# Optimization experiments

Hardware: AMD Instinct MI355X
Metric: run time of the kernel (lower is better)

Reference implementation:

```python
import jax, jax.numpy as jnp
import numpy as np

T, N, FIN, HID, E = 3, 50000, 4, 128, 1600000
EPS = 1e-5


def setup_inputs() -> dict:
    key = jax.random.key(0)
    ks = jax.random.split(key, 16)
    s = 0.05
    return {
        "X": jax.random.normal(ks[0], (T, N, FIN), jnp.float32),
        "edge_index": jax.random.randint(ks[1], (2, E), 0, N, jnp.int64),
        "edge_weight": jax.random.uniform(ks[2], (E,), jnp.float32),
        "w1": jax.random.normal(ks[3], (FIN, HID), jnp.float32) * s,
        "wc": jax.random.normal(ks[4], (3, HID, HID), jnp.float32) * s,
        "bc": jnp.zeros((4, HID), jnp.float32),
        "bn_gamma": jnp.ones((4, HID), jnp.float32),
        "bn_beta": jnp.zeros((4, HID), jnp.float32),
        "lstm_wih": jax.random.normal(ks[5], (2, 4 * HID, HID), jnp.float32) * s,
        "lstm_whh": jax.random.normal(ks[6], (2, 4 * HID, HID), jnp.float32) * s,
        "lstm_b": jnp.zeros((2, 4 * HID), jnp.float32),
        "lin1_w": jax.random.normal(ks[7], (HID + T, HID), jnp.float32) * s,
        "lin1_b": jnp.zeros((HID,), jnp.float32),
        "lin2_w": jax.random.normal(ks[8], (HID, 1), jnp.float32) * s,
        "lin2_b": jnp.zeros((1,), jnp.float32),
    }


def reference(X, edge_index, edge_weight, w1, wc, bc, bn_gamma, bn_beta,
              lstm_wih, lstm_whh, lstm_b, lin1_w, lin1_b, lin2_w, lin2_b):
    n = X.shape[1]
    src, dst = edge_index[0], edge_index[1]
    loop = jnp.arange(n)
    # PyG gcn_norm: add self loops (weight 1), symmetric normalization
    src_a = jnp.concatenate([src, loop])
    dst_a = jnp.concatenate([dst, loop])
    w_a = jnp.concatenate([edge_weight, jnp.ones((n,), X.dtype)])
    deg = jax.ops.segment_sum(w_a, dst_a, num_segments=n)
    dinv = jnp.where(deg > 0, deg ** -0.5, 0.0)
    norm = dinv[src_a] * w_a * dinv[dst_a]  # [E+N]

    def gcn(x, w, b):
        h = x @ w                                   # [N,H] transform first (F small)
        msg = h[src_a] * norm[:, None]              # gather + scale
        return jax.ops.segment_sum(msg, dst_a, num_segments=n) + b

    def bn(h, g, beta):  # BatchNorm1d with batch stats (track_running_stats=False)
        mu = h.mean(0)
        var = ((h - mu) ** 2).mean(0)
        return (h - mu) / jnp.sqrt(var + EPS) * g + beta

    def per_timestep(x):
        h = bn(jax.nn.relu(gcn(x, w1, bc[0])), bn_gamma[0], bn_beta[0])
        for i in range(3):
            h = bn(jax.nn.relu(gcn(h, wc[i], bc[i + 1])), bn_gamma[i + 1], bn_beta[i + 1])
        return h

    C = jax.vmap(per_timestep)(X)  # [T, N, H]

    def lstm_layer(seq, wih, whh, b):
        hdim = whh.shape[1]
        h0 = jnp.zeros((seq.shape[1], hdim), seq.dtype)

        def step(carry, x):
            h, c = carry
            gates = x @ wih.T + h @ whh.T + b
            i, f, g, o = jnp.split(gates, 4, axis=-1)  # torch gate order i,f,g,o
            c = jax.nn.sigmoid(f) * c + jax.nn.sigmoid(i) * jnp.tanh(g)
            h = jax.nn.sigmoid(o) * jnp.tanh(c)
            return (h, c), h

        (hT, _), ys = jax.lax.scan(step, (h0, h0), seq)
        return ys, hT

    seq = C
    for layer in range(2):
        seq, hT = lstm_layer(seq, lstm_wih[layer], lstm_whh[layer], lstm_b[layer])

    h = jax.nn.relu(hT)                 # last layer's final hidden, [N, H]
    S = X[:, :, 0].T                    # [N, T]
    h = jnp.concatenate([h, S], axis=-1)
    h = h @ lin1_w + lin1_b
    h = h @ lin2_w + lin2_b             # dropout is identity at inference
    return h
```

## Files before the change

### kernel.cpp

```cpp
#include <hip/hip_runtime.h>
#include <hip/hip_fp8.h>
#include <cstdint>

#define TT  3
#define FIN 4
#define HID 128
#define RS16 384
#define RS32 192
#define RS8  384

typedef unsigned int   u32;
typedef unsigned short u16;
typedef unsigned char  u8;
typedef unsigned long long u64;
typedef float f32x2 __attribute__((ext_vector_type(2)));
typedef float f32x4 __attribute__((ext_vector_type(4)));
typedef __bf16 bf16x8 __attribute__((ext_vector_type(8)));

static __device__ __forceinline__ f32x4 mfma_bf16(bf16x8 a, bf16x8 b, f32x4 c) {
  return __builtin_amdgcn_mfma_f32_16x16x32_bf16(a, b, c, 0, 0, 0);
}
static __device__ __forceinline__ float sigf(float v) { return 1.f / (1.f + expf(-v)); }
static __device__ __forceinline__ float bf_lo(u32 u) { return __uint_as_float(u << 16); }
static __device__ __forceinline__ float bf_hi(u32 u) { return __uint_as_float(u & 0xffff0000u); }
static __device__ __forceinline__ u16 bfbits(float f) {
  return __builtin_bit_cast(unsigned short, (__bf16)f);
}
static __device__ __forceinline__ u8 f_to_fp8(float f) {
  __hip_fp8_e4m3 v(f); return (u8)v.__x;
}
static __device__ __forceinline__ f32x2 fp8x2_to_f32(u16 x) {
  return __builtin_amdgcn_cvt_pk_f32_fp8((int)(u32)x, false);
}


__global__ void k_init(u64* pk, float* stats, int* ticket, int n) {
  int i = blockIdx.x * 256 + threadIdx.x;
  if (i < n) pk[i] = 0ull;
  if (blockIdx.x == 0) {
    for (int k = 0; k < 3; ++k) stats[k * 256 + threadIdx.x] = 0.f;
    if (threadIdx.x == 0) *ticket = 0;
  }
}

__global__ void k_deg(const int* __restrict__ dstv, const float* __restrict__ ew,
                      u64* pk, int* __restrict__ epos, int E_) {
  int e = blockIdx.x * 256 + threadIdx.x;
  if (e < E_) {
    int d = dstv[e];
    u64 inc = (1ull << 42) | (u64)(ew[e] * 4294967296.0f);
    u64 old = atomicAdd(&pk[d], inc);
    epos[e] = (int)(old >> 42);
  }
}

__global__ __launch_bounds__(256) void k_scanA(const u64* __restrict__ pk, int* rowptr,
    int* partial, float* dinv, float* selfn, int n) {
  __shared__ int wsum[4];
  int tid = threadIdx.x, lane = tid & 63, wv = tid >> 6;
  int i = blockIdx.x * 256 + tid;
  int v = 0;
  if (i < n) {
    u64 p = pk[i];
    v = (int)(p >> 42);
    float degw = (float)((double)(p & ((1ull << 42) - 1)) * (1.0 / 4294967296.0) + 1.0);
    float r = rsqrtf(degw);
    dinv[i] = r; selfn[i] = r * r;
  }
  int inc = v;
  #pragma unroll
  for (int off = 1; off < 64; off <<= 1) {
    int t2 = __shfl_up(inc, off);
    if (lane >= off) inc += t2;
  }
  if (lane == 63) wsum[wv] = inc;
  __syncthreads();
  if (tid == 0) {
    int s = 0;
    #pragma unroll
    for (int j = 0; j < 4; ++j) { int t3 = wsum[j]; wsum[j] = s; s += t3; }
    partial[blockIdx.x] = s;
  }
  __syncthreads();
  int excl = wsum[wv] + inc - v;
  if (i <= n) rowptr[i] = excl;
}

__global__ __launch_bounds__(256) void k_scanB(int* partial, int nb) {
  __shared__ int wsum[4];
  int tid = threadIdx.x, lane = tid & 63, wv = tid >> 6;
  int v = (tid < nb) ? partial[tid] : 0;
  int inc = v;
  #pragma unroll
  for (int off = 1; off < 64; off <<= 1) {
    int t2 = __shfl_up(inc, off);
    if (lane >= off) inc += t2;
  }
  if (lane == 63) wsum[wv] = inc;
  __syncthreads();
  if (tid == 0) {
    int s = 0;
    #pragma unroll
    for (int j = 0; j < 4; ++j) { int t3 = wsum[j]; wsum[j] = s; s += t3; }
  }
  __syncthreads();
  int excl = wsum[wv] + inc - v;
  if (tid < nb) partial[tid] = excl;
}

__global__ void k_scanC(int* rowptr, const int* __restrict__ partial, int n) {
  int i = blockIdx.x * 256 + threadIdx.x;
  if (i <= n) rowptr[i] += partial[blockIdx.x];
}

__global__ void k_fillcsr(const int* __restrict__ srcv, const int* __restrict__ dstv,
                          const float* __restrict__ ew, const float* __restrict__ dinv,
                          const int* __restrict__ rowptr, const int* __restrict__ epos,
                          int2* __restrict__ csr, int E_) {
  int e = blockIdx.x * 256 + threadIdx.x;
  if (e < E_) {
    int d = dstv[e], s = srcv[e];
    int idx = rowptr[d] + epos[e];
    csr[idx] = make_int2(s, __float_as_int(dinv[s] * ew[e] * dinv[d]));
  }
}


__global__ __launch_bounds__(256) void k_aggX(const float* __restrict__ X,
    const int* __restrict__ rowptr, const int2* __restrict__ csr,
    const float* __restrict__ selfn, float* __restrict__ XA, int N_) {
  int wv = threadIdx.x >> 6, l = threadIdx.x & 63;
  int wid = blockIdx.x * 4 + wv, nw = gridDim.x * 4;
  for (int n = wid; n < N_; n += nw) {
    float acc[12];
    #pragma unroll
    for (int i = 0; i < 12; ++i) acc[i] = 0.f;
    int e0 = rowptr[n], e1 = rowptr[n + 1];
    for (int e = e0 + l; e < e1; e += 64) {
      int2 v2 = csr[e];
      int s = v2.x; float wn = __int_as_float(v2.y);
      #pragma unroll
      for (int t = 0; t < TT; ++t) {
        float4 v = *(const float4*)(X + ((size_t)t * N_ + s) * FIN);
        acc[t*4+0] += wn * v.x; acc[t*4+1] += wn * v.y;
        acc[t*4+2] += wn * v.z; acc[t*4+3] += wn * v.w;
      }
    }
    #pragma unroll
    for (int i = 0; i < 12; ++i)
      for (int off = 32; off; off >>= 1) acc[i] += __shfl_down(acc[i], off);
    if (l == 0) {
      float sn = selfn[n];
      #pragma unroll
      for (int t = 0; t < TT; ++t) {
        float4 v = *(const float4*)(X + ((size_t)t * N_ + n) * FIN);
        XA[(size_t)n*12 + t*4+0] = acc[t*4+0] + sn * v.x;
        XA[(size_t)n*12 + t*4+1] = acc[t*4+1] + sn * v.y;
        XA[(size_t)n*12 + t*4+2] = acc[t*4+2] + sn * v.z;
        XA[(size_t)n*12 + t*4+3] = acc[t*4+3] + sn * v.w;
      }
    }
  }
}

__global__ void k_l0c(const float* __restrict__ XA, const float* __restrict__ w1,
                      const float* __restrict__ bc0, u32* __restrict__ out32, int N_) {
  int tid = blockIdx.x * 256 + threadIdx.x;
  if (tid >= N_ * 64) return;
  int n = tid >> 6, l = tid & 63, cp = 2 * l;
  float w00 = w1[cp],       w01 = w1[cp+1];
  float w10 = w1[HID+cp],   w11 = w1[HID+cp+1];
  float w20 = w1[2*HID+cp], w21 = w1[2*HID+cp+1];
  float w30 = w1[3*HID+cp], w31 = w1[3*HID+cp+1];
  float b0 = bc0[cp], b1 = bc0[cp+1];
  const float* xa = XA + (size_t)n * 12;
  u32* orow = out32 + (size_t)n * RS32 + l;
  #pragma unroll
  for (int t = 0; t < TT; ++t) {
    float4 x = *(const float4*)(xa + t * 4);
    float v0 = fmaxf(b0 + x.x*w00 + x.y*w10 + x.z*w20 + x.w*w30, 0.f);
    float v1 = fmaxf(b1 + x.x*w01 + x.y*w11 + x.z*w21 + x.w*w31, 0.f);
    orow[t * 64] = (u32)bfbits(v0) | ((u32)bfbits(v1) << 16);
  }
}


__global__ __launch_bounds__(256) void k_stats3(const u32* __restrict__ H32, float* stats,
    int* ticket, const float* __restrict__ gamma, const float* __restrict__ beta,
    float* aff , int N_) {
  __shared__ float red[256][12];
  __shared__ int lastf;
  int l = threadIdx.x & 63, half = threadIdx.x >> 6;
  float s1[TT][2] = {}, s2[TT][2] = {};
  for (int n = blockIdx.x * 4 + half; n < N_; n += gridDim.x * 4) {
    const u32* row = H32 + (size_t)n * RS32 + l;
    #pragma unroll
    for (int t = 0; t < TT; ++t) {
      u32 u = row[t * 64];
      float v0 = bf_lo(u), v1 = bf_hi(u);
      s1[t][0] += v0; s2[t][0] += v0 * v0;
      s1[t][1] += v1; s2[t][1] += v1 * v1;
    }
  }
  #pragma unroll
  for (int t = 0; t < TT; ++t) {
    red[threadIdx.x][t*4+0] = s1[t][0]; red[threadIdx.x][t*4+1] = s2[t][0];
    red[threadIdx.x][t*4+2] = s1[t][1]; red[threadIdx.x][t*4+3] = s2[t][1];
  }
  __syncthreads();
  if (half == 0) {
    #pragma unroll
    for (int t = 0; t < TT; ++t) {
      float a0 = 0, a1 = 0, a2 = 0, a3 = 0;
      #pragma unroll
      for (int h2 = 0; h2 < 4; ++h2) {
        a0 += red[h2*64 + l][t*4+0]; a1 += red[h2*64 + l][t*4+1];
        a2 += red[h2*64 + l][t*4+2]; a3 += red[h2*64 + l][t*4+3];
      }
      atomicAdd(&stats[t*256 + 2*l], a0);       atomicAdd(&stats[t*256 + 128 + 2*l], a1);
      atomicAdd(&stats[t*256 + 2*l + 1], a2);   atomicAdd(&stats[t*256 + 128 + 2*l + 1], a3);
    }
  }
  __syncthreads();
  if (threadIdx.x == 0) {
    __threadfence();
    int tk = __hip_atomic_fetch_add(ticket, 1, __ATOMIC_ACQ_REL, __HIP_MEMORY_SCOPE_AGENT);
    lastf = (tk == (int)gridDim.x - 1) ? 1 : 0;
  }
  __syncthreads();
  if (lastf) {
    float invn = 1.f / (float)N_;
    for (int i = threadIdx.x; i < 384; i += 256) {
      int t = i >> 7, c = i & 127;
      float s1v = __hip_atomic_load(&stats[t*256 + c],       __ATOMIC_RELAXED, __HIP_MEMORY_SCOPE_AGENT);
      float s2v = __hip_atomic_load(&stats[t*256 + 128 + c], __ATOMIC_RELAXED, __HIP_MEMORY_SCOPE_AGENT);
      float mu = s1v * invn;
      float var = fmaxf(s2v * invn - mu * mu, 0.f);
      float a = gamma[c] * rsqrtf(var + 1e-5f);
      aff[t*256 + c] = a;
      aff[t*256 + 128 + c] = beta[c] - mu * a;
      stats[t*256 + c] = 0.f; stats[t*256 + 128 + c] = 0.f;
    }
    if (threadIdx.x == 0) *ticket = 0;
  }
}


__global__ void k_swzall(const float* __restrict__ wc, const float* __restrict__ wih,
                         const float* __restrict__ whh,
                         bf16x8* __restrict__ wcsw, bf16x8* __restrict__ wstk) {
  int id = blockIdx.x * 256 + threadIdx.x;
  if (id < 6144) {
    int i = id >> 11, lid = id & 2047;
    int l = lid & 63, frag = lid >> 6;
    int cb = frag & 7, kb = frag >> 3;
    int col = cb * 16 + (l & 15);
    int k0 = kb * 32 + (l >> 4) * 8;
    const float* W = wc + (size_t)i * HID * HID;
    bf16x8 v;
    #pragma unroll
    for (int j = 0; j < 8; ++j) v[j] = (__bf16)W[(size_t)(k0 + j) * HID + col];
    wcsw[i * 2048 + lid] = v;
  } else if (id < 6144 + 32768) {
    int id2 = id - 6144;
    int layer = id2 >> 14, lid = id2 & 16383;
    int l = lid & 63, frag = lid >> 6;
    int cb = frag & 31, kb = frag >> 5;
    int col = cb * 16 + (l & 15);
    int k0 = kb * 32 + (l >> 4) * 8;
    const float* wi = wih + (size_t)layer * 512 * HID;
    const float* wh = whh + (size_t)layer * 512 * HID;
    bf16x8 v;
    #pragma unroll
    for (int j = 0; j < 8; ++j) {
      int k = k0 + j;
      float val = (k < HID) ? wi[(size_t)col * HID + k] : wh[(size_t)col * HID + (k - HID)];
      v[j] = (__bf16)val;
    }
    wstk[layer * 16384 + lid] = v;
  }
}

__global__ void k_headprep(const float* __restrict__ l1w, const float* __restrict__ l1b,
                           const float* __restrict__ l2w, const float* __restrict__ l2b,
                           float* __restrict__ hw) {
  int k = threadIdx.x;
  if (k < HID + TT) {
    float s = 0.f;
    for (int j = 0; j < HID; ++j) s += l1w[(size_t)k * HID + j] * l2w[j];
    hw[k] = s;
  } else if (k == HID + TT) {
    float s = l2b[0];
    for (int j = 0; j < HID; ++j) s += l1b[j] * l2w[j];
    hw[HID + TT] = s;
  }
}


__global__ __launch_bounds__(256) void k_trans3(const u16* __restrict__ Xin,
    const float* __restrict__ aff, const bf16x8* __restrict__ wsw,
    u8* __restrict__ Y, int nblk, int N_) {
  int w = threadIdx.x >> 6, l = threadIdx.x & 63;
  int lr = l & 15, lk = l >> 4;
  int t = blockIdx.x / nblk;
  int blk = blockIdx.x - t * nblk;
  int rbase = blk * 64 + w * 16;
  int arow = rbase + lr;
  bool av = arow < N_;
  const float* fa = aff + t * 256;
  const float* fb = fa + 128;
  f32x4 acc[8];
  #pragma unroll
  for (int cb = 0; cb < 8; ++cb) acc[cb] = (f32x4){0.f, 0.f, 0.f, 0.f};
  #pragma unroll
  for (int kb = 0; kb < 4; ++kb) {
    int ko = kb * 32 + lk * 8;
    bf16x8 af;
    if (av) {
      uint4 u = *(const uint4*)(Xin + (size_t)arow * RS16 + t * 128 + ko);
      float4 a0 = *(const float4*)(fa + ko), a1 = *(const float4*)(fa + ko + 4);
      float4 b0 = *(const float4*)(fb + ko), b1 = *(const float4*)(fb + ko + 4);
      af[0] = (__bf16)(bf_lo(u.x) * a0.x + b0.x);
      af[1] = (__bf16)(bf_hi(u.x) * a0.y + b0.y);
      af[2] = (__bf16)(bf_lo(u.y) * a0.z + b0.z);
      af[3] = (__bf16)(bf_hi(u.y) * a0.w + b0.w);
      af[4] = (__bf16)(bf_lo(u.z) * a1.x + b1.x);
      af[5] = (__bf16)(bf_hi(u.z) * a1.y + b1.y);
      af[6] = (__bf16)(bf_lo(u.w) * a1.z + b1.z);
      af[7] = (__bf16)(bf_hi(u.w) * a1.w + b1.w);
    } else {
      #pragma unroll
      for (int j = 0; j < 8; ++j) af[j] = (__bf16)0.f;
    }
    #pragma unroll
    for (int cb = 0; cb < 8; ++cb) {
      bf16x8 bf = wsw[(kb * 8 + cb) * 64 + l];
      acc[cb] = mfma_bf16(af, bf, acc[cb]);
    }
  }
  #pragma unroll
  for (int cb = 0; cb < 8; ++cb)
    #pragma unroll
    for (int i2 = 0; i2 < 4; ++i2) {
      int orow = rbase + lk * 4 + i2;
      if (orow < N_)
        Y[(size_t)orow * RS8 + t * 128 + cb * 16 + lr] = f_to_fp8(acc[cb][i2]);
    }
}


__global__ __launch_bounds__(256) void k_agg3(const u8* __restrict__ H8,
    const int* __restrict__ rowptr, const int2* __restrict__ csr,
    const float* __restrict__ selfn, const float* __restrict__ bias,
    u16* __restrict__ outp, int N_) {
  int wv = threadIdx.x >> 6, l = threadIdx.x & 63;
  int wid = blockIdx.x * 4 + wv, nw = gridDim.x * 4;
  float b0 = bias[2 * l], b1 = bias[2 * l + 1];
  u32* O32 = (u32*)outp;
  for (int n = wid; n < N_; n += nw) {
    const u16* self = (const u16*)(H8 + (size_t)n * RS8) + l;
    float sn = selfn[n];
    f32x2 v0 = fp8x2_to_f32(self[0]);
    f32x2 v1 = fp8x2_to_f32(self[64]);
    f32x2 v2 = fp8x2_to_f32(self[128]);
    float a00 = sn * v0.x, a01 = sn * v0.y;
    float a10 = sn * v1.x, a11 = sn * v1.y;
    float a20 = sn * v2.x, a21 = sn * v2.y;
    int e0 = rowptr[n], e1 = rowptr[n + 1];
    int e = e0;
    for (; e + 7 < e1; e += 8) {
      int2 c[8];
      #pragma unroll
      for (int j = 0; j < 8; ++j) c[j] = csr[e + j];
      u16 x[8][3];
      #pragma unroll
      for (int j = 0; j < 8; ++j) {
        const u16* p = (const u16*)(H8 + (size_t)c[j].x * RS8) + l;
        x[j][0] = p[0]; x[j][1] = p[64]; x[j][2] = p[128];
      }
      #pragma unroll
      for (int j = 0; j < 8; ++j) {
        float w = __int_as_float(c[j].y);
        f32x2 y0 = fp8x2_to_f32(x[j][0]);
        f32x2 y1 = fp8x2_to_f32(x[j][1]);
        f32x2 y2 = fp8x2_to_f32(x[j][2]);
        a00 += w * y0.x; a01 += w * y0.y;
        a10 += w * y1.x; a11 += w * y1.y;
        a20 += w * y2.x; a21 += w * y2.y;
      }
    }
    for (; e < e1; ++e) {
      int2 c0 = csr[e];
      const u16* p = (const u16*)(H8 + (size_t)c0.x * RS8) + l;
      float w = __int_as_float(c0.y);
      f32x2 y0 = fp8x2_to_f32(p[0]);
      f32x2 y1 = fp8x2_to_f32(p[64]);
      f32x2 y2 = fp8x2_to_f32(p[128]);
      a00 += w * y0.x; a01 += w * y0.y;
      a10 += w * y1.x; a11 += w * y1.y;
      a20 += w * y2.x; a21 += w * y2.y;
    }
    u32* orow = O32 + (size_t)n * RS32 + l;
    orow[0]   = (u32)bfbits(fmaxf(a00 + b0, 0.f)) | ((u32)bfbits(fmaxf(a01 + b1, 0.f)) << 16);
    orow[64]  = (u32)bfbits(fmaxf(a10 + b0, 0.f)) | ((u32)bfbits(fmaxf(a11 + b1, 0.f)) << 16);
    orow[128] = (u32)bfbits(fmaxf(a20 + b0, 0.f)) | ((u32)bfbits(fmaxf(a21 + b1, 0.f)) << 16);
  }
}


__global__ __launch_bounds__(256) void k_lstm(
    const u16* __restrict__ xb, int xs, const u16* __restrict__ hpb,
    const float* __restrict__ aff,
    float* __restrict__ cstate, u16* __restrict__ hout,
    const bf16x8* __restrict__ wsw, const float* __restrict__ bias,
    int first, int N_) {
  __shared__ __bf16 gl[32][512];
  int w = threadIdx.x >> 6, l = threadIdx.x & 63;
  int lr = l & 15, lk = l >> 4;
  int r0 = blockIdx.x * 32;
  f32x4 acc[2][8];
  #pragma unroll
  for (int rb = 0; rb < 2; ++rb)
    #pragma unroll
    for (int cb = 0; cb < 8; ++cb) acc[rb][cb] = (f32x4){0.f, 0.f, 0.f, 0.f};

  #pragma unroll
  for (int kb = 0; kb < 4; ++kb) {
    int ko = kb * 32 + lk * 8;
    bf16x8 af[2];
    #pragma unroll
    for (int rb = 0; rb < 2; ++rb) {
      int row = r0 + rb * 16 + lr;
      if (row < N_) {
        uint4 u = *(const uint4*)(xb + (size_t)row * xs + ko);
        if (aff) {
          float4 a0 = *(const float4*)(aff + ko),       a1 = *(const float4*)(aff + ko + 4);
          float4 b0 = *(const float4*)(aff + HID + ko), b1 = *(const float4*)(aff + HID + ko + 4);
          af[rb][0] = (__bf16)(bf_lo(u.x) * a0.x + b0.x);
          af[rb][1] = (__bf16)(bf_hi(u.x) * a0.y + b0.y);
          af[rb][2] = (__bf16)(bf_lo(u.y) * a0.z + b0.z);
          af[rb][3] = (__bf16)(bf_hi(u.y) * a0.w + b0.w);
          af[rb][4] = (__bf16)(bf_lo(u.z) * a1.x + b1.x);
          af[rb][5] = (__bf16)(bf_hi(u.z) * a1.y + b1.y);
          af[rb][6] = (__bf16)(bf_lo(u.w) * a1.z + b1.z);
          af[rb][7] = (__bf16)(bf_hi(u.w) * a1.w + b1.w);
        } else {
          af[rb] = __builtin_bit_cast(bf16x8, u);
        }
      } else {
        #pragma unroll
        for (int j = 0; j < 8; ++j) af[rb][j] = (__bf16)0.f;
      }
    }
    #pragma unroll
    for (int cb = 0; cb < 8; ++cb) {
      bf16x8 bf = wsw[(kb * 32 + w * 8 + cb) * 64 + l];
      acc[0][cb] = mfma_bf16(af[0], bf, acc[0][cb]);
      acc[1][cb] = mfma_bf16(af[1], bf, acc[1][cb]);
    }
  }
  if (!first) {
    #pragma unroll
    for (int kb = 0; kb < 4; ++kb) {
      int ko = kb * 32 + lk * 8;
      bf16x8 af[2];
      #pragma unroll
      for (int rb = 0; rb < 2; ++rb) {
        int row = r0 + rb * 16 + lr;
        if (row < N_) {
          af[rb] = __builtin_bit_cast(bf16x8, *(const uint4*)(hpb + (size_t)row * HID + ko));
        } else {
          #pragma unroll
          for (int j = 0; j < 8; ++j) af[rb][j] = (__bf16)0.f;
        }
      }
      #pragma unroll
      for (int cb = 0; cb < 8; ++cb) {
        bf16x8 bf = wsw[((kb + 4) * 32 + w * 8 + cb) * 64 + l];
        acc[0][cb] = mfma_bf16(af[0], bf, acc[0][cb]);
        acc[1][cb] = mfma_bf16(af[1], bf, acc[1][cb]);
      }
    }
  }
  #pragma unroll
  for (int rb = 0; rb < 2; ++rb)
    #pragma unroll
    for (int cb = 0; cb < 8; ++cb)
      #pragma unroll
      for (int i2 = 0; i2 < 4; ++i2)
        gl[rb * 16 + lk * 4 + i2][w * 128 + cb * 16 + lr] = (__bf16)acc[rb][cb][i2];
  __syncthreads();
  for (int it = threadIdx.x; it < 32 * HID; it += 256) {
    int nl = it >> 7, j = it & 127;
    int n = r0 + nl;
    if (n >= N_) continue;
    float ig = (float)gl[nl][j]       + bias[j];
    float fg = (float)gl[nl][128 + j] + bias[128 + j];
    float gg = (float)gl[nl][256 + j] + bias[256 + j];
    float og = (float)gl[nl][384 + j] + bias[384 + j];
    float cp = first ? 0.f : cstate[(size_t)n * HID + j];
    float cn = sigf(fg) * cp + sigf(ig) * tanhf(gg);
    float hn = sigf(og) * tanhf(cn);
    cstate[(size_t)n * HID + j] = cn;
    hout[(size_t)n * HID + j] = bfbits(hn);
  }
}


__global__ __launch_bounds__(256) void k_final2(const u32* __restrict__ H2,
    const float* __restrict__ Xin, const float* __restrict__ hw,
    float* __restrict__ outp, int N_) {
  int wv = threadIdx.x >> 6, l = threadIdx.x & 63;
  int wid = blockIdx.x * 4 + wv, nw = gridDim.x * 4;
  float wc0 = hw[2 * l], wc1 = hw[2 * l + 1];
  float ws0 = hw[HID], ws1 = hw[HID + 1], ws2 = hw[HID + 2], bb = hw[HID + 3];
  for (int n = wid; n < N_; n += nw) {
    u32 u = H2[(size_t)n * 64 + l];
    float p = fmaxf(bf_lo(u), 0.f) * wc0 + fmaxf(bf_hi(u), 0.f) * wc1;
    #pragma unroll
    for (int off = 32; off; off >>= 1) p += __shfl_down(p, off);
    if (l == 0) {
      p += Xin[(size_t)n * FIN] * ws0
         + Xin[((size_t)N_ + n) * FIN] * ws1
         + Xin[((size_t)2 * N_ + n) * FIN] * ws2;
      outp[n] = p + bb;
    }
  }
}


extern "C" void kernel_launch(void* const* d_in, const int* in_sizes, int n_in,
                              void* d_out, int out_size, void* d_ws, size_t ws_size,
                              hipStream_t stream) {
  const float* X   = (const float*)d_in[0];
  const int*   ei  = (const int*)  d_in[1];
  const float* ew  = (const float*)d_in[2];
  const float* w1  = (const float*)d_in[3];
  const float* wc  = (const float*)d_in[4];
  const float* bc  = (const float*)d_in[5];
  const float* gam = (const float*)d_in[6];
  const float* bet = (const float*)d_in[7];
  const float* wih = (const float*)d_in[8];
  const float* whh = (const float*)d_in[9];
  const float* lb  = (const float*)d_in[10];
  const float* l1w = (const float*)d_in[11];
  const float* l1b = (const float*)d_in[12];
  const float* l2w = (const float*)d_in[13];
  const float* l2b = (const float*)d_in[14];
  float* outp = (float*)d_out;
  (void)n_in; (void)out_size; (void)ws_size;

  const int N = in_sizes[0] / (TT * FIN);
  const int E = in_sizes[1] / 2;
  const int* srcv = ei;
  const int* dstv = ei + E;

  char* base = (char*)d_ws;
  size_t off = 0;
  auto alloc = [&](size_t b) -> void* {
    void* p = base + off;
    off += (b + 255) & ~(size_t)255;
    return p;
  };

  u64*   pk     = (u64*)  alloc((size_t)N * 8);
  int*   epos   = (int*)  alloc((size_t)E * 4);
  int*   rowptr = (int*)  alloc(((size_t)N + 1) * 4);
  int*   partial= (int*)  alloc(1024);
  float* dinv   = (float*)alloc((size_t)N * 4);
  float* selfn  = (float*)alloc((size_t)N * 4);
  int2*  csr    = (int2*) alloc((size_t)E * 8);
  float* XA     = (float*)alloc((size_t)N * 12 * 4);
  u16*   Ga     = (u16*)  alloc((size_t)N * RS16 * 2);
  u16*   Gb     = (u16*)  alloc((size_t)N * RS16 * 2);
  u8*    Htb    = (u8*)   alloc((size_t)N * RS8);
  u16*   Gcat   = (u16*)  alloc((size_t)N * RS16 * 2);
  float* stats  = (float*)alloc(768 * 4);
  int*   ticket = (int*)  alloc(256);
  float* affA   = (float*)alloc((size_t)3 * 256 * 4);
  float* aff3   = (float*)alloc((size_t)3 * 256 * 4);
  float* hw     = (float*)alloc(136 * 4);
  bf16x8* wcsw  = (bf16x8*)alloc((size_t)3 * 2048 * 16);
  bf16x8* wstk  = (bf16x8*)alloc((size_t)2 * 16384 * 16);
  u16*   Cb     = Ga;
  float* cbuf   = (float*)Gb;

  int gN = (N + 255) / 256, gE = (E + 255) / 256;
  int nb = (N + 255) / 256;
  int nblk = (N + 63) / 64;

  k_init<<<gN, 256, 0, stream>>>(pk, stats, ticket, N);
  k_deg<<<gE, 256, 0, stream>>>(dstv, ew, pk, epos, E);
  k_scanA<<<nb, 256, 0, stream>>>(pk, rowptr, partial, dinv, selfn, N);
  k_scanB<<<1, 256, 0, stream>>>(partial, nb);
  k_scanC<<<nb, 256, 0, stream>>>(rowptr, partial, N);
  k_fillcsr<<<gE, 256, 0, stream>>>(srcv, dstv, ew, dinv, rowptr, epos, csr, E);
  k_aggX<<<1024, 256, 0, stream>>>(X, rowptr, csr, selfn, XA, N);
  k_swzall<<<152, 256, 0, stream>>>(wc, wih, whh, wcsw, wstk);
  k_headprep<<<1, 256, 0, stream>>>(l1w, l1b, l2w, l2b, hw);

  k_l0c<<<(N * 64 + 255) / 256, 256, 0, stream>>>(XA, w1, bc, (u32*)Ga, N);
  k_stats3<<<256, 256, 0, stream>>>((const u32*)Ga, stats, ticket, gam, bet, affA, N);

  k_trans3<<<3 * nblk, 256, 0, stream>>>(Ga, affA, wcsw, Htb, nblk, N);
  k_agg3<<<2048, 256, 0, stream>>>(Htb, rowptr, csr, selfn, bc + HID, Gb, N);
  k_stats3<<<256, 256, 0, stream>>>((const u32*)Gb, stats, ticket, gam + HID, bet + HID, affA, N);

  k_trans3<<<3 * nblk, 256, 0, stream>>>(Gb, affA, wcsw + 2048, Htb, nblk, N);
  k_agg3<<<2048, 256, 0, stream>>>(Htb, rowptr, csr, selfn, bc + 2 * HID, Gb, N);
  k_stats3<<<256, 256, 0, stream>>>((const u32*)Gb, stats, ticket, gam + 2 * HID, bet + 2 * HID, affA, N);

  k_trans3<<<3 * nblk, 256, 0, stream>>>(Gb, affA, wcsw + 4096, Htb, nblk, N);
  k_agg3<<<2048, 256, 0, stream>>>(Htb, rowptr, csr, selfn, bc + 3 * HID, Gcat, N);
  k_stats3<<<256, 256, 0, stream>>>((const u32*)Gcat, stats, ticket, gam + 3 * HID, bet + 3 * HID, aff3, N);

  int gL = (N + 31) / 32;
  for (int t = 0; t < TT; ++t) {
    u16* Ct = Cb + (size_t)t * N * HID;
    const u16* hp = (t == 0) ? Ct : (Cb + (size_t)(t - 1) * N * HID);
    k_lstm<<<gL, 256, 0, stream>>>(Gcat + (size_t)t * HID, RS16, hp,
                                   aff3 + (size_t)t * 256, cbuf, Ct,
                                   wstk, lb, (t == 0) ? 1 : 0, N);
  }
  for (int t = 0; t < TT; ++t) {
    u16* Ct = Cb + (size_t)t * N * HID;
    const u16* hp = (t == 0) ? Ct : (Cb + (size_t)(t - 1) * N * HID);
    k_lstm<<<gL, 256, 0, stream>>>(Ct, HID, hp, nullptr, cbuf, Ct,
                                   wstk + 16384, lb + 512, (t == 0) ? 1 : 0, N);
  }
  k_final2<<<512, 256, 0, stream>>>((const u32*)(Cb + (size_t)2 * N * HID), X, hw, outp, N);
}
```

Measured before the change: 1.074 ms.

## Fuse LSTM timesteps into one kernel per layer with on-chip h/c state

Each LSTM layer now runs all three timesteps in a single kernel. The hidden and cell state stay in shared memory between steps instead of going through global buffers. This removes four kernel launches and the global read/write of c and h_prev per step, and the first layer writes its full sequence while the second writes only the final hidden state. Separately, the fp8 gather-aggregate loop is unrolled by 4 instead of 8, which lowers register pressure at the cost of fewer gathers in flight.

```diff
diff --git a/kernel.cpp b/kernel.cpp
--- a/kernel.cpp
+++ b/kernel.cpp
@@ -368,26 +368,31 @@
     float a20 = sn * v2.x, a21 = sn * v2.y;
     int e0 = rowptr[n], e1 = rowptr[n + 1];
     int e = e0;
-    for (; e + 7 < e1; e += 8) {
-      int2 c[8];
-      #pragma unroll
-      for (int j = 0; j < 8; ++j) c[j] = csr[e + j];
-      u16 x[8][3];
-      #pragma unroll
-      for (int j = 0; j < 8; ++j) {
-        const u16* p = (const u16*)(H8 + (size_t)c[j].x * RS8) + l;
-        x[j][0] = p[0]; x[j][1] = p[64]; x[j][2] = p[128];
-      }
-      #pragma unroll
-      for (int j = 0; j < 8; ++j) {
-        float w = __int_as_float(c[j].y);
-        f32x2 y0 = fp8x2_to_f32(x[j][0]);
-        f32x2 y1 = fp8x2_to_f32(x[j][1]);
-        f32x2 y2 = fp8x2_to_f32(x[j][2]);
-        a00 += w * y0.x; a01 += w * y0.y;
-        a10 += w * y1.x; a11 += w * y1.y;
-        a20 += w * y2.x; a21 += w * y2.y;
-      }
+    for (; e + 3 < e1; e += 4) {
+      int2 c0 = csr[e], c1 = csr[e+1], c2 = csr[e+2], c3 = csr[e+3];
+      const u16* p0 = (const u16*)(H8 + (size_t)c0.x * RS8) + l;
+      const u16* p1 = (const u16*)(H8 + (size_t)c1.x * RS8) + l;
+      const u16* p2 = (const u16*)(H8 + (size_t)c2.x * RS8) + l;
+      const u16* p3 = (const u16*)(H8 + (size_t)c3.x * RS8) + l;
+      u16 x00 = p0[0], x01 = p0[64], x02 = p0[128];
+      u16 x10 = p1[0], x11 = p1[64], x12 = p1[128];
+      u16 x20 = p2[0], x21 = p2[64], x22 = p2[128];
+      u16 x30 = p3[0], x31 = p3[64], x32 = p3[128];
+      float w0 = __int_as_float(c0.y), w1v = __int_as_float(c1.y);
+      float w2 = __int_as_float(c2.y), w3v = __int_as_float(c3.y);
+      f32x2 y;
+      y = fp8x2_to_f32(x00); a00 += w0 * y.x; a01 += w0 * y.y;
+      y = fp8x2_to_f32(x10); a00 += w1v * y.x; a01 += w1v * y.y;
+      y = fp8x2_to_f32(x20); a00 += w2 * y.x; a01 += w2 * y.y;
+      y = fp8x2_to_f32(x30); a00 += w3v * y.x; a01 += w3v * y.y;
+      y = fp8x2_to_f32(x01); a10 += w0 * y.x; a11 += w0 * y.y;
+      y = fp8x2_to_f32(x11); a10 += w1v * y.x; a11 += w1v * y.y;
+      y = fp8x2_to_f32(x21); a10 += w2 * y.x; a11 += w2 * y.y;
+      y = fp8x2_to_f32(x31); a10 += w3v * y.x; a11 += w3v * y.y;
+      y = fp8x2_to_f32(x02); a20 += w0 * y.x; a21 += w0 * y.y;
+      y = fp8x2_to_f32(x12); a20 += w1v * y.x; a21 += w1v * y.y;
+      y = fp8x2_to_f32(x22); a20 += w2 * y.x; a21 += w2 * y.y;
+      y = fp8x2_to_f32(x32); a20 += w3v * y.x; a21 += w3v * y.y;
     }
     for (; e < e1; ++e) {
       int2 c0 = csr[e];
@@ -408,58 +413,28 @@
 }
 
 
-__global__ __launch_bounds__(256) void k_lstm(
-    const u16* __restrict__ xb, int xs, const u16* __restrict__ hpb,
-    const float* __restrict__ aff,
-    float* __restrict__ cstate, u16* __restrict__ hout,
-    const bf16x8* __restrict__ wsw, const float* __restrict__ bias,
-    int first, int N_) {
+__global__ __launch_bounds__(256) void k_lstm3(
+    const u16* __restrict__ xb, int xrs, int xts,
+    const float* __restrict__ aff3,
+    u16* __restrict__ hout, int hts, int writeAll,
+    const bf16x8* __restrict__ wsw, const float* __restrict__ bias, int N_) {
   __shared__ __bf16 gl[32][512];
+  __shared__ __bf16 hl[32][136];
+  __shared__ float  cl[32][132];
   int w = threadIdx.x >> 6, l = threadIdx.x & 63;
   int lr = l & 15, lk = l >> 4;
   int r0 = blockIdx.x * 32;
-  f32x4 acc[2][8];
-  #pragma unroll
-  for (int rb = 0; rb < 2; ++rb)
-    #pragma unroll
-    for (int cb = 0; cb < 8; ++cb) acc[rb][cb] = (f32x4){0.f, 0.f, 0.f, 0.f};
-
-  #pragma unroll
-  for (int kb = 0; kb < 4; ++kb) {
-    int ko = kb * 32 + lk * 8;
-    bf16x8 af[2];
-    #pragma unroll
-    for (int rb = 0; rb < 2; ++rb) {
-      int row = r0 + rb * 16 + lr;
-      if (row < N_) {
-        uint4 u = *(const uint4*)(xb + (size_t)row * xs + ko);
-        if (aff) {
-          float4 a0 = *(const float4*)(aff + ko),       a1 = *(const float4*)(aff + ko + 4);
-          float4 b0 = *(const float4*)(aff + HID + ko), b1 = *(const float4*)(aff + HID + ko + 4);
-          af[rb][0] = (__bf16)(bf_lo(u.x) * a0.x + b0.x);
-          af[rb][1] = (__bf16)(bf_hi(u.x) * a0.y + b0.y);
-          af[rb][2] = (__bf16)(bf_lo(u.y) * a0.z + b0.z);
-          af[rb][3] = (__bf16)(bf_hi(u.y) * a0.w + b0.w);
-          af[rb][4] = (__bf16)(bf_lo(u.z) * a1.x + b1.x);
-          af[rb][5] = (__bf16)(bf_hi(u.z) * a1.y + b1.y);
-          af[rb][6] = (__bf16)(bf_lo(u.w) * a1.z + b1.z);
-          af[rb][7] = (__bf16)(bf_hi(u.w) * a1.w + b1.w);
-        } else {
-          af[rb] = __builtin_bit_cast(bf16x8, u);
-        }
-      } else {
-        #pragma unroll
-        for (int j = 0; j < 8; ++j) af[rb][j] = (__bf16)0.f;
-      }
-    }
-    #pragma unroll
-    for (int cb = 0; cb < 8; ++cb) {
-      bf16x8 bf = wsw[(kb * 32 + w * 8 + cb) * 64 + l];
-      acc[0][cb] = mfma_bf16(af[0], bf, acc[0][cb]);
-      acc[1][cb] = mfma_bf16(af[1], bf, acc[1][cb]);
-    }
-  }
-  if (!first) {
+
+  #pragma unroll 1
+  for (int t = 0; t < TT; ++t) {
+    const u16* xt = xb + (size_t)t * xts;
+    const float* aff = aff3 ? (aff3 + (size_t)t * 256) : nullptr;
+    f32x4 acc[2][8];
+    #pragma unroll
+    for (int rb = 0; rb < 2; ++rb)
+      #pragma unroll
+      for (int cb = 0; cb < 8; ++cb) acc[rb][cb] = (f32x4){0.f, 0.f, 0.f, 0.f};
+
     #pragma unroll
     for (int kb = 0; kb < 4; ++kb) {
       int ko = kb * 32 + lk * 8;
@@ -468,7 +443,21 @@
       for (int rb = 0; rb < 2; ++rb) {
         int row = r0 + rb * 16 + lr;
         if (row < N_) {
-          af[rb] = __builtin_bit_cast(bf16x8, *(const uint4*)(hpb + (size_t)row * HID + ko));
+          uint4 u = *(const uint4*)(xt + (size_t)row * xrs + ko);
+          if (aff) {
+            float4 a0 = *(const float4*)(aff + ko),       a1 = *(const float4*)(aff + ko + 4);
+            float4 b0 = *(const float4*)(aff + HID + ko), b1 = *(const float4*)(aff + HID + ko + 4);
+            af[rb][0] = (__bf16)(bf_lo(u.x) * a0.x + b0.x);
+            af[rb][1] = (__bf16)(bf_hi(u.x) * a0.y + b0.y);
+            af[rb][2] = (__bf16)(bf_lo(u.y) * a0.z + b0.z);
+            af[rb][3] = (__bf16)(bf_hi(u.y) * a0.w + b0.w);
+            af[rb][4] = (__bf16)(bf_lo(u.z) * a1.x + b1.x);
+            af[rb][5] = (__bf16)(bf_hi(u.z) * a1.y + b1.y);
+            af[rb][6] = (__bf16)(bf_lo(u.w) * a1.z + b1.z);
+            af[rb][7] = (__bf16)(bf_hi(u.w) * a1.w + b1.w);
+          } else {
+            af[rb] = __builtin_bit_cast(bf16x8, u);
+          }
         } else {
           #pragma unroll
           for (int j = 0; j < 8; ++j) af[rb][j] = (__bf16)0.f;
@@ -476,33 +465,52 @@
       }
       #pragma unroll
       for (int cb = 0; cb < 8; ++cb) {
-        bf16x8 bf = wsw[((kb + 4) * 32 + w * 8 + cb) * 64 + l];
+        bf16x8 bf = wsw[(kb * 32 + w * 8 + cb) * 64 + l];
         acc[0][cb] = mfma_bf16(af[0], bf, acc[0][cb]);
         acc[1][cb] = mfma_bf16(af[1], bf, acc[1][cb]);
       }
     }
-  }
-  #pragma unroll
-  for (int rb = 0; rb < 2; ++rb)
-    #pragma unroll
-    for (int cb = 0; cb < 8; ++cb)
-      #pragma unroll
-      for (int i2 = 0; i2 < 4; ++i2)
-        gl[rb * 16 + lk * 4 + i2][w * 128 + cb * 16 + lr] = (__bf16)acc[rb][cb][i2];
-  __syncthreads();
-  for (int it = threadIdx.x; it < 32 * HID; it += 256) {
-    int nl = it >> 7, j = it & 127;
-    int n = r0 + nl;
-    if (n >= N_) continue;
-    float ig = (float)gl[nl][j]       + bias[j];
-    float fg = (float)gl[nl][128 + j] + bias[128 + j];
-    float gg = (float)gl[nl][256 + j] + bias[256 + j];
-    float og = (float)gl[nl][384 + j] + bias[384 + j];
-    float cp = first ? 0.f : cstate[(size_t)n * HID + j];
-    float cn = sigf(fg) * cp + sigf(ig) * tanhf(gg);
-    float hn = sigf(og) * tanhf(cn);
-    cstate[(size_t)n * HID + j] = cn;
-    hout[(size_t)n * HID + j] = bfbits(hn);
+    if (t > 0) {
+      #pragma unroll
+      for (int kb = 0; kb < 4; ++kb) {
+        int ko = kb * 32 + lk * 8;
+        bf16x8 af[2];
+        #pragma unroll
+        for (int rb = 0; rb < 2; ++rb)
+          af[rb] = *(const bf16x8*)&hl[rb * 16 + lr][ko];
+        #pragma unroll
+        for (int cb = 0; cb < 8; ++cb) {
+          bf16x8 bf = wsw[((kb + 4) * 32 + w * 8 + cb) * 64 + l];
+          acc[0][cb] = mfma_bf16(af[0], bf, acc[0][cb]);
+          acc[1][cb] = mfma_bf16(af[1], bf, acc[1][cb]);
+        }
+      }
+    }
+    #pragma unroll
+    for (int rb = 0; rb < 2; ++rb)
+      #pragma unroll
+      for (int cb = 0; cb < 8; ++cb)
+        #pragma unroll
+        for (int i2 = 0; i2 < 4; ++i2)
+          gl[rb * 16 + lk * 4 + i2][w * 128 + cb * 16 + lr] = (__bf16)acc[rb][cb][i2];
+    __syncthreads();
+
+    for (int it = threadIdx.x; it < 32 * HID; it += 256) {
+      int nl = it >> 7, j = it & 127;
+      int n = r0 + nl;
+      float ig = (float)gl[nl][j]       + bias[j];
+      float fg = (float)gl[nl][128 + j] + bias[128 + j];
+      float gg = (float)gl[nl][256 + j] + bias[256 + j];
+      float og = (float)gl[nl][384 + j] + bias[384 + j];
+      float cp = (t > 0) ? cl[nl][j] : 0.f;
+      float cn = sigf(fg) * cp + sigf(ig) * tanhf(gg);
+      float hn = sigf(og) * tanhf(cn);
+      cl[nl][j] = cn;
+      hl[nl][j] = (__bf16)hn;
+      if (n < N_ && (writeAll || t == TT - 1))
+        hout[(size_t)t * hts + (size_t)n * HID + j] = bfbits(hn);
+    }
+    __syncthreads();
   }
 }
 
@@ -582,8 +590,8 @@
   float* hw     = (float*)alloc(136 * 4);
   bf16x8* wcsw  = (bf16x8*)alloc((size_t)3 * 2048 * 16);
   bf16x8* wstk  = (bf16x8*)alloc((size_t)2 * 16384 * 16);
-  u16*   Cb     = Ga;
-  float* cbuf   = (float*)Gb;
+  u16*   H1     = Gb;
+  u16*   H2f    = Ga;
 
   int gN = (N + 255) / 256, gE = (E + 255) / 256;
   int nb = (N + 255) / 256;
@@ -615,18 +623,10 @@
   k_stats3<<<256, 256, 0, stream>>>((const u32*)Gcat, stats, ticket, gam + 3 * HID, bet + 3 * HID, aff3, N);
 
   int gL = (N + 31) / 32;
-  for (int t = 0; t < TT; ++t) {
-    u16* Ct = Cb + (size_t)t * N * HID;
-    const u16* hp = (t == 0) ? Ct : (Cb + (size_t)(t - 1) * N * HID);
-    k_lstm<<<gL, 256, 0, stream>>>(Gcat + (size_t)t * HID, RS16, hp,
-                                   aff3 + (size_t)t * 256, cbuf, Ct,
-                                   wstk, lb, (t == 0) ? 1 : 0, N);
-  }
-  for (int t = 0; t < TT; ++t) {
-    u16* Ct = Cb + (size_t)t * N * HID;
-    const u16* hp = (t == 0) ? Ct : (Cb + (size_t)(t - 1) * N * HID);
-    k_lstm<<<gL, 256, 0, stream>>>(Ct, HID, hp, nullptr, cbuf, Ct,
-                                   wstk + 16384, lb + 512, (t == 0) ? 1 : 0, N);
-  }
-  k_final2<<<512, 256, 0, stream>>>((const u32*)(Cb + (size_t)2 * N * HID), X, hw, outp, N);
-}
+  k_lstm3<<<gL, 256, 0, stream>>>(Gcat, RS16, HID, aff3,
+                                  H1, N * HID, 1, wstk, lb, N);
+  k_lstm3<<<gL, 256, 0, stream>>>(H1, HID, N * HID, nullptr,
+                                  H2f, 0, 0, wstk + 16384, lb + 512, N);
+
+  k_final2<<<512, 256, 0, stream>>>((const u32*)H2f, X, hw, outp, N);
+}
```

Measured after the change: 1.219 ms. +13.4%, slower.
